# Optimization experiments

Hardware: AMD Instinct MI355X
Metric: run time of the kernel (lower is better)

The kernel has to match this reference:

```python
import jax, jax.numpy as jnp
import numpy as np

N, E, B, D = 50000, 800000, 250, 128
EPS = 1e-5


def setup_inputs() -> dict:
    key = jax.random.key(0)
    ks = jax.random.split(key, 12)
    x = jax.random.normal(ks[0], (N, D), jnp.float32)
    w = jax.random.uniform(ks[1], (E, 4), jnp.float32)
    src = jax.random.randint(ks[2], (E,), 0, N)
    dst = jax.random.randint(ks[3], (E,), 0, N)
    graph_ids = jnp.sort(jax.random.randint(ks[4], (N,), 0, B))
    s = 1.0 / np.sqrt(D)
    W1 = jax.random.normal(ks[5], (D, D), jnp.float32) * s
    W2 = jax.random.normal(ks[6], (D, D), jnp.float32) * s
    W3 = jax.random.normal(ks[7], (D, D), jnp.float32) * s
    ln1_g = jnp.ones((D,), jnp.float32)
    ln1_b = jnp.zeros((D,), jnp.float32)
    ln2_g = jnp.ones((D,), jnp.float32)
    ln2_b = jnp.zeros((D,), jnp.float32)
    return dict(x=x, w=w, W1=W1, W2=W2, W3=W3, ln1_g=ln1_g, ln1_b=ln1_b,
                ln2_g=ln2_g, ln2_b=ln2_b, src=src, dst=dst, graph_ids=graph_ids)


def _layernorm(h, g, b):
    mu = jnp.mean(h, axis=-1, keepdims=True)
    var = jnp.mean(jnp.square(h - mu), axis=-1, keepdims=True)
    return (h - mu) * jax.lax.rsqrt(var + EPS) * g + b


def reference(x, w, W1, W2, W3, ln1_g, ln1_b, ln2_g, ln2_b, src, dst, graph_ids):
    # edge feature [E,Fe] -> scalar edge weight [E] (mean over feature dim)
    w_s = jnp.mean(w, axis=-1)
    ones_e = jnp.ones((E,), x.dtype)
    # DGL norm='both': unweighted degrees, clamped to >= 1
    out_deg = jnp.clip(jax.ops.segment_sum(ones_e, src, num_segments=N), 1.0)
    in_deg = jnp.clip(jax.ops.segment_sum(ones_e, dst, num_segments=N), 1.0)
    out_norm = jax.lax.rsqrt(out_deg)[:, None]  # [N,1]
    in_norm = jax.lax.rsqrt(in_deg)[:, None]    # [N,1]

    def gconv(h, W):
        m = (h * out_norm)[src] * w_s[:, None]                 # [E,D] gather-mul
        agg = jax.ops.segment_sum(m, dst, num_segments=N)      # [N,D] scatter-add
        return (agg * in_norm) @ W                              # [N,D_out]

    h = _layernorm(jax.nn.relu(gconv(x, W1)), ln1_g, ln1_b)
    h = _layernorm(jax.nn.relu(gconv(h, W2)), ln2_g, ln2_b)
    h = gconv(h, W3)
    # per-graph segmented sum readout -> [B, D]
    return jax.ops.segment_sum(h, graph_ids, num_segments=B)
```

## Files before the change

kernel.cpp:

```cpp
#include <hip/hip_runtime.h>

#define D 128
#define RS 16
#define NBMAX 1024
constexpr float EPS = 1e-5f;

typedef short bf16x8 __attribute__((ext_vector_type(8)));
typedef float f32x4 __attribute__((ext_vector_type(4)));
typedef unsigned long long u64;

__device__ __forceinline__ uint f2bf(float f) {
  union { float f; uint u; } v; v.f = f;
  return (v.u + 0x7fffu + ((v.u >> 16) & 1u)) >> 16;
}
__device__ __forceinline__ float bflo(uint u) {
  union { uint u; float f; } v; v.u = u << 16; return v.f;
}
__device__ __forceinline__ float bfhi(uint u) {
  union { uint u; float f; } v; v.u = u & 0xffff0000u; return v.f;
}

__device__ __forceinline__ int lower_bound(const int* __restrict__ a, int n, int key) {
  int lo = 0, hi = n;
  while (lo < hi) { int m = (lo + hi) >> 1; if (a[m] < key) lo = m + 1; else hi = m; }
  return lo;
}

__global__ __launch_bounds__(256) void k_pre(
    const int* __restrict__ src, const int* __restrict__ dst,
    int* __restrict__ ocnt, int* __restrict__ btot, int E, int nb, int ebA,
    const float4* __restrict__ x, uint4* __restrict__ xb, int n8, int cb,
    const float* __restrict__ W1, const float* __restrict__ W2,
    const float* __restrict__ W3, ushort* __restrict__ Wf) {
  __shared__ int hloc[NBMAX];
  int bid = blockIdx.x;
  int tid = threadIdx.x;
  if (bid < ebA) {
    for (int j = tid; j < nb; j += 256) hloc[j] = 0;
    __syncthreads();
    int e0 = bid * 4096;
#pragma unroll 4
    for (int it = 0; it < 16; ++it) {
      int e = e0 + it * 256 + tid;
      if (e < E) {
        atomicAdd(&ocnt[src[e]], 1);
        atomicAdd(&hloc[dst[e] >> 6], 1);
      }
    }
    __syncthreads();
    for (int j = tid; j < nb; j += 256) {
      int c = hloc[j];
      if (c) atomicAdd(&btot[j], c);
    }
  } else if (bid < ebA + cb) {
    int i = (bid - ebA) * 256 + tid;
    if (i < n8) {
      float4 p = x[i * 2], q = x[i * 2 + 1];
      uint4 o;
      o.x = f2bf(p.x) | (f2bf(p.y) << 16);
      o.y = f2bf(p.z) | (f2bf(p.w) << 16);
      o.z = f2bf(q.x) | (f2bf(q.y) << 16);
      o.w = f2bf(q.z) | (f2bf(q.w) << 16);
      xb[i] = o;
    }
  } else {
    int t4 = (bid - ebA - cb) * 256 + tid;
    if (t4 < 3 * 2048) {
      const float* Wsrc = (t4 < 2048) ? W1 : (t4 < 4096) ? W2 : W3;
      int t = t4 & 2047;
      int lane = t & 63;
      int frag = t >> 6;
      int ks = frag >> 3, ct = frag & 7;
      int col = ct * 16 + (lane & 15);
      int kb = ks * 32 + (lane >> 4) * 8;
      uint p[8];
#pragma unroll
      for (int j = 0; j < 8; ++j) p[j] = f2bf(Wsrc[(kb + j) * D + col]);
      uint4 o;
      o.x = p[0] | (p[1] << 16);
      o.y = p[2] | (p[3] << 16);
      o.z = p[4] | (p[5] << 16);
      o.w = p[6] | (p[7] << 16);
      *(uint4*)(Wf + (size_t)t4 * 8) = o;
    }
  }
}

__global__ void k_onorm(const int* __restrict__ ocnt, float* __restrict__ outn, int N) {
  int n = blockIdx.x * 256 + threadIdx.x;
  if (n < N) outn[n] = rsqrtf(fmaxf((float)ocnt[n], 1.0f));
}

__global__ __launch_bounds__(1024) void k_bbase(const int* __restrict__ btot,
                                                int* __restrict__ bb,
                                                int* __restrict__ rowptr,
                                                int nb, int E, int N) {
  __shared__ int part[1024];
  int t = threadIdx.x;
  int v = (t < nb) ? btot[t] : 0;
  part[t] = v;
  __syncthreads();
  for (int off = 1; off < 1024; off <<= 1) {
    int u = (t >= off) ? part[t - off] : 0;
    __syncthreads();
    part[t] += u;
    __syncthreads();
  }
  if (t < nb) bb[t] = part[t] - v;
  if (t == 0) { bb[nb] = E; rowptr[N] = E; }
}

__global__ __launch_bounds__(256) void k_bscatter(
    const int* __restrict__ src, const int* __restrict__ dst,
    const float4* __restrict__ w, const float* __restrict__ outn,
    const int* __restrict__ bb, int* __restrict__ bcur,
    u64* __restrict__ ebuf, int E, int nb) {
  __shared__ int hloc[NBMAX];
  __shared__ int hcur[NBMAX];
  int bid = blockIdx.x, tid = threadIdx.x;
  for (int j = tid; j < nb; j += 256) hloc[j] = 0;
  __syncthreads();
  int e0 = bid * 4096;
#pragma unroll 4
  for (int it = 0; it < 16; ++it) {
    int e = e0 + it * 256 + tid;
    if (e < E) atomicAdd(&hloc[dst[e] >> 6], 1);
  }
  __syncthreads();
  for (int j = tid; j < nb; j += 256) {
    int c = hloc[j];
    hcur[j] = c ? (bb[j] + atomicAdd(&bcur[j], c)) : 0;
  }
  __syncthreads();
#pragma unroll 4
  for (int it = 0; it < 16; ++it) {
    int e = e0 + it * 256 + tid;
    if (e < E) {
      int d = dst[e], s = src[e];
      int pos = atomicAdd(&hcur[d >> 6], 1);
      float4 wv = w[e];
      float coef = (wv.x + wv.y + wv.z + wv.w) * 0.25f * outn[s];
      u64 pk = ((u64)__float_as_uint(coef) << 32) |
               ((u64)(d & 63) << 16) | (uint)s;
      ebuf[pos] = pk;
    }
  }
}

__global__ __launch_bounds__(256) void k_bplace(
    const u64* __restrict__ ebuf, const int* __restrict__ bb,
    int* __restrict__ rowptr, float* __restrict__ innm,
    u64* __restrict__ ecsr, int N) {
  __shared__ int c64[64], ex[64], cur[64];
  int b = blockIdx.x, tid = threadIdx.x;
  int base = bb[b];
  int cnt = bb[b + 1] - base;
  if (tid < 64) c64[tid] = 0;
  __syncthreads();
  for (int i = tid; i < cnt; i += 256) {
    u64 v = ebuf[base + i];
    atomicAdd(&c64[(int)((v >> 16) & 63)], 1);
  }
  __syncthreads();
  if (tid < 64) {
    int cv = c64[tid];
    int inc = cv;
#pragma unroll
    for (int off = 1; off < 64; off <<= 1) {
      int u = __shfl_up(inc, off);
      if (tid >= off) inc += u;
    }
    int excl = inc - cv;
    ex[tid] = excl;
    cur[tid] = 0;
    int node = b * 64 + tid;
    if (node < N) {
      rowptr[node] = base + excl;
      innm[node] = rsqrtf(fmaxf((float)cv, 1.0f));
    }
  }
  __syncthreads();
  for (int i = tid; i < cnt; i += 256) {
    u64 v = ebuf[base + i];
    int dl = (int)((v >> 16) & 63);
    int pos = base + ex[dl] + atomicAdd(&cur[dl], 1);
    ecsr[pos] = (v & 0xFFFFFFFF00000000ull) | (v & 0xFFFFull);
  }
}

__global__ __launch_bounds__(256) void k_fused(
    const ushort* __restrict__ h, const int* __restrict__ rowptr,
    const u64* __restrict__ ecsr,
    const float* __restrict__ innm, const ushort* __restrict__ Wf,
    const float* __restrict__ g, const float* __restrict__ bta,
    void* __restrict__ out, int N, int do_ln) {
  __shared__ float lds[4][16 * D];
  const int lane = threadIdx.x & 63;
  const int wv = threadIdx.x >> 6;
  const int row0 = blockIdx.x * 64 + wv * 16;
  if (row0 >= N) return;

  ushort* at = (ushort*)&lds[wv][0];
  {
    const int grp = lane >> 4;
    const int c = lane & 15;
    for (int rr = 0; rr < 4; ++rr) {
      int n = row0 + grp * 4 + rr;
      if (n >= N) break;
      int beg = rowptr[n], end = rowptr[n + 1];
      float a0 = 0, a1 = 0, a2 = 0, a3 = 0, a4 = 0, a5 = 0, a6 = 0, a7 = 0;
#define ACC8(q, f)                                          \
  a0 = fmaf(bflo(q.x), f, a0); a1 = fmaf(bfhi(q.x), f, a1); \
  a2 = fmaf(bflo(q.y), f, a2); a3 = fmaf(bfhi(q.y), f, a3); \
  a4 = fmaf(bflo(q.z), f, a4); a5 = fmaf(bfhi(q.z), f, a5); \
  a6 = fmaf(bflo(q.w), f, a6); a7 = fmaf(bfhi(q.w), f, a7);
      int j = beg;
      for (; j + 4 <= end; j += 4) {
        u64 v0 = ecsr[j], v1 = ecsr[j + 1], v2 = ecsr[j + 2], v3 = ecsr[j + 3];
        const ushort* p0 = h + (size_t)(v0 & 0xFFFFu) * D + c * 8;
        const ushort* p1 = h + (size_t)(v1 & 0xFFFFu) * D + c * 8;
        const ushort* p2 = h + (size_t)(v2 & 0xFFFFu) * D + c * 8;
        const ushort* p3 = h + (size_t)(v3 & 0xFFFFu) * D + c * 8;
        float f0 = __uint_as_float((uint)(v0 >> 32));
        float f1 = __uint_as_float((uint)(v1 >> 32));
        float f2 = __uint_as_float((uint)(v2 >> 32));
        float f3 = __uint_as_float((uint)(v3 >> 32));
        uint4 q0 = *(const uint4*)p0;
        uint4 q1 = *(const uint4*)p1;
        uint4 q2 = *(const uint4*)p2;
        uint4 q3 = *(const uint4*)p3;
        ACC8(q0, f0) ACC8(q1, f1) ACC8(q2, f2) ACC8(q3, f3)
      }
      for (; j < end; ++j) {
        u64 v = ecsr[j];
        float f = __uint_as_float((uint)(v >> 32));
        uint4 q = *(const uint4*)(h + (size_t)(v & 0xFFFFu) * D + c * 8);
        ACC8(q, f)
      }
#undef ACC8
      float sc = innm[n];
      uint4 o;
      o.x = f2bf(a0 * sc) | (f2bf(a1 * sc) << 16);
      o.y = f2bf(a2 * sc) | (f2bf(a3 * sc) << 16);
      o.z = f2bf(a4 * sc) | (f2bf(a5 * sc) << 16);
      o.w = f2bf(a6 * sc) | (f2bf(a7 * sc) << 16);
      *(uint4*)(at + (grp * 4 + rr) * 136 + c * 8) = o;
    }
  }
  asm volatile("s_waitcnt lgkmcnt(0)" ::: "memory");
  __builtin_amdgcn_sched_barrier(0);

  const int lc = lane & 15, lg = lane >> 4;
  f32x4 acc[8];
#pragma unroll
  for (int ct = 0; ct < 8; ++ct) acc[ct] = (f32x4){0.f, 0.f, 0.f, 0.f};
#pragma unroll
  for (int ks = 0; ks < 4; ++ks) {
    bf16x8 a = *(const bf16x8*)(at + lc * 136 + ks * 32 + lg * 8);
    const ushort* wp = Wf + ((size_t)(ks * 8) * 64 + lane) * 8;
#pragma unroll
    for (int ct = 0; ct < 8; ++ct) {
      bf16x8 b = *(const bf16x8*)(wp + ct * 512);
      acc[ct] = __builtin_amdgcn_mfma_f32_16x16x32_bf16(a, b, acc[ct], 0, 0, 0);
    }
  }
  asm volatile("s_waitcnt lgkmcnt(0)" ::: "memory");
  __builtin_amdgcn_sched_barrier(0);

  if (do_ln) {
    float v[8][4];
#pragma unroll
    for (int ct = 0; ct < 8; ++ct)
#pragma unroll
      for (int j = 0; j < 4; ++j) v[ct][j] = fmaxf(acc[ct][j], 0.f);
    float mu[4], rs[4];
#pragma unroll
    for (int j = 0; j < 4; ++j) {
      float s = 0.f;
#pragma unroll
      for (int ct = 0; ct < 8; ++ct) s += v[ct][j];
#pragma unroll
      for (int off = 1; off < 16; off <<= 1) s += __shfl_xor(s, off);
      mu[j] = s * (1.0f / D);
    }
#pragma unroll
    for (int j = 0; j < 4; ++j) {
      float q = 0.f;
#pragma unroll
      for (int ct = 0; ct < 8; ++ct) {
        v[ct][j] -= mu[j];
        q = fmaf(v[ct][j], v[ct][j], q);
      }
#pragma unroll
      for (int off = 1; off < 16; off <<= 1) q += __shfl_xor(q, off);
      rs[j] = rsqrtf(q * (1.0f / D) + EPS);
    }
    ushort* lp = (ushort*)&lds[wv][0];
#pragma unroll
    for (int ct = 0; ct < 8; ++ct) {
      float gc = g[ct * 16 + lc], bc = bta[ct * 16 + lc];
#pragma unroll
      for (int j = 0; j < 4; ++j)
        lp[(lg * 4 + j) * D + ct * 16 + lc] = (ushort)f2bf(fmaf(v[ct][j] * rs[j], gc, bc));
    }
    __builtin_amdgcn_wave_barrier();
    int r = row0 + (lane >> 2);
    if (r < N) {
      ushort* ob = (ushort*)out + (size_t)row0 * D + lane * 32;
#pragma unroll
      for (int i = 0; i < 4; ++i)
        ((uint4*)ob)[i] = ((const uint4*)(lp + lane * 32))[i];
    }
  } else {
    float* lp = &lds[wv][0];
#pragma unroll
    for (int ct = 0; ct < 8; ++ct)
#pragma unroll
      for (int j = 0; j < 4; ++j)
        lp[(lg * 4 + j) * D + ct * 16 + lc] = acc[ct][j];
    __builtin_amdgcn_wave_barrier();
    int r = row0 + (lane >> 2);
    if (r < N) {
      float* ob = (float*)out + (size_t)row0 * D + lane * 32;
#pragma unroll
      for (int i = 0; i < 8; ++i)
        ((float4*)ob)[i] = ((const float4*)(lp + lane * 32))[i];
    }
  }
}

__global__ __launch_bounds__(128) void k_rpart(
    const float* __restrict__ h, const int* __restrict__ gid,
    float* __restrict__ part, int N) {
  int b = blockIdx.x / RS, s = blockIdx.x % RS;
  int t = threadIdx.x;
  int start = lower_bound(gid, N, b);
  int end = lower_bound(gid, N, b + 1);
  int len = end - start;
  int chunk = (len + RS - 1) / RS;
  int rb = start + s * chunk;
  int re = min(rb + chunk, end);
  float acc = 0.f;
  for (int n = rb; n < re; ++n) acc += h[(size_t)n * D + t];
  part[((size_t)b * RS + s) * D + t] = acc;
}

__global__ __launch_bounds__(128) void k_rsum(
    const float* __restrict__ part, float* __restrict__ out) {
  int b = blockIdx.x;
  int t = threadIdx.x;
  float acc = 0.f;
#pragma unroll
  for (int s = 0; s < RS; ++s) acc += part[((size_t)b * RS + s) * D + t];
  out[(size_t)b * D + t] = acc;
}

extern "C" void kernel_launch(void* const* d_in, const int* in_sizes, int n_in,
                              void* d_out, int out_size, void* d_ws, size_t ws_size,
                              hipStream_t stream) {
  const float* x    = (const float*)d_in[0];
  const float* w    = (const float*)d_in[1];
  const float* W1   = (const float*)d_in[2];
  const float* W2   = (const float*)d_in[3];
  const float* W3   = (const float*)d_in[4];
  const float* ln1g = (const float*)d_in[5];
  const float* ln1b = (const float*)d_in[6];
  const float* ln2g = (const float*)d_in[7];
  const float* ln2b = (const float*)d_in[8];
  const int* src = (const int*)d_in[9];
  const int* dst = (const int*)d_in[10];
  const int* gid = (const int*)d_in[11];
  const int N = in_sizes[0] / D;
  const int E = in_sizes[9];
  const int B = out_size / D;
  float* outp = (float*)d_out;

  float*  h3f  = (float*)d_ws;
  ushort* xb   = (ushort*)(h3f + (size_t)N * D);
  ushort* hb1  = xb + (size_t)N * D;
  ushort* Wf   = hb1 + (size_t)N * D;
  float*  outn = (float*)(Wf + 3 * 2048 * 8);
  float*  innm = outn + N;
  const int nb  = (N + 63) >> 6;
  const int ebA = (E + 4095) / 4096;
  int*    ocnt = (int*)(innm + N);
  int*    btot = ocnt + N;
  int*    bcur = btot + nb;
  int*    rowptr = bcur + nb;
  int*    bb   = rowptr + N + 2;
  u64*    ecsr = (u64*)(bb + nb + 2);
  float*  part = (float*)(ecsr + E);
  u64*    ebuf = (u64*)h3f;

  const int mb  = (N + 63) / 64;
  const int n8  = N * D / 8;
  const int cb  = (n8 + 255) / 256;

  hipMemsetAsync(ocnt, 0, sizeof(int) * ((size_t)N + 2 * nb), stream);
  k_pre<<<ebA + cb + 24, 256, 0, stream>>>(src, dst, ocnt, btot, E, nb, ebA,
                                           (const float4*)x, (uint4*)xb, n8, cb,
                                           W1, W2, W3, Wf);
  k_onorm<<<(N + 255) / 256, 256, 0, stream>>>(ocnt, outn, N);
  k_bbase<<<1, 1024, 0, stream>>>(btot, bb, rowptr, nb, E, N);
  k_bscatter<<<ebA, 256, 0, stream>>>(src, dst, (const float4*)w, outn, bb, bcur,
                                      ebuf, E, nb);
  k_bplace<<<nb, 256, 0, stream>>>(ebuf, bb, rowptr, innm, ecsr, N);

  k_fused<<<mb, 256, 0, stream>>>(xb, rowptr, ecsr, innm, Wf,
                                  ln1g, ln1b, hb1, N, 1);
  k_fused<<<mb, 256, 0, stream>>>(hb1, rowptr, ecsr, innm, Wf + 16384,
                                  ln2g, ln2b, xb, N, 1);
  k_fused<<<mb, 256, 0, stream>>>(xb, rowptr, ecsr, innm, Wf + 32768,
                                  nullptr, nullptr, h3f, N, 0);

  k_rpart<<<B * RS, 128, 0, stream>>>(h3f, gid, part, N);
  k_rsum<<<B, 128, 0, stream>>>(part, outp);
}
```

Baseline: 221.4 us.

## Replace global out-degree atomics with bucketed source histogram and per-bucket counting

Out-degrees were counted with 800K global atomics on per-node counters. Now source IDs are bucketed by node>>6 using LDS histograms, the same way destinations are. A second scatter writes the bucketed source IDs and a new k_scount kernel counts them per node in LDS. The out-norm multiply moves from k_bscatter into k_bplace. This removes contended global atomics and the k_onorm launch, but adds an extra scatter pass of 3.2MB, another kernel and a second prefix scan.

```diff
diff --git a/kernel.cpp b/kernel.cpp
--- a/kernel.cpp
+++ b/kernel.cpp
@@ -28,29 +28,32 @@
 
 __global__ __launch_bounds__(256) void k_pre(
     const int* __restrict__ src, const int* __restrict__ dst,
-    int* __restrict__ ocnt, int* __restrict__ btot, int E, int nb, int ebA,
+    int* __restrict__ btot, int* __restrict__ btot2, int E, int nb, int ebA,
     const float4* __restrict__ x, uint4* __restrict__ xb, int n8, int cb,
     const float* __restrict__ W1, const float* __restrict__ W2,
     const float* __restrict__ W3, ushort* __restrict__ Wf) {
-  __shared__ int hloc[NBMAX];
+  __shared__ int hd[NBMAX];
+  __shared__ int hs[NBMAX];
   int bid = blockIdx.x;
   int tid = threadIdx.x;
   if (bid < ebA) {
-    for (int j = tid; j < nb; j += 256) hloc[j] = 0;
+    for (int j = tid; j < nb; j += 256) { hd[j] = 0; hs[j] = 0; }
     __syncthreads();
     int e0 = bid * 4096;
 #pragma unroll 4
     for (int it = 0; it < 16; ++it) {
       int e = e0 + it * 256 + tid;
       if (e < E) {
-        atomicAdd(&ocnt[src[e]], 1);
-        atomicAdd(&hloc[dst[e] >> 6], 1);
+        atomicAdd(&hd[dst[e] >> 6], 1);
+        atomicAdd(&hs[src[e] >> 6], 1);
       }
     }
     __syncthreads();
     for (int j = tid; j < nb; j += 256) {
-      int c = hloc[j];
-      if (c) atomicAdd(&btot[j], c);
+      int cd = hd[j];
+      if (cd) atomicAdd(&btot[j], cd);
+      int cs = hs[j];
+      if (cs) atomicAdd(&btot2[j], cs);
     }
   } else if (bid < ebA + cb) {
     int i = (bid - ebA) * 256 + tid;
@@ -86,15 +89,10 @@
   }
 }
 
-__global__ void k_onorm(const int* __restrict__ ocnt, float* __restrict__ outn, int N) {
-  int n = blockIdx.x * 256 + threadIdx.x;
-  if (n < N) outn[n] = rsqrtf(fmaxf((float)ocnt[n], 1.0f));
-}
-
-__global__ __launch_bounds__(1024) void k_bbase(const int* __restrict__ btot,
-                                                int* __restrict__ bb,
-                                                int* __restrict__ rowptr,
-                                                int nb, int E, int N) {
+__global__ __launch_bounds__(1024) void k_bbase(
+    const int* __restrict__ btot, const int* __restrict__ btot2,
+    int* __restrict__ bb, int* __restrict__ bb2,
+    int* __restrict__ rowptr, int nb, int E, int N) {
   __shared__ int part[1024];
   int t = threadIdx.x;
   int v = (t < nb) ? btot[t] : 0;
@@ -108,28 +106,46 @@
   }
   if (t < nb) bb[t] = part[t] - v;
   if (t == 0) { bb[nb] = E; rowptr[N] = E; }
+  __syncthreads();
+  int v2 = (t < nb) ? btot2[t] : 0;
+  part[t] = v2;
+  __syncthreads();
+  for (int off = 1; off < 1024; off <<= 1) {
+    int u = (t >= off) ? part[t - off] : 0;
+    __syncthreads();
+    part[t] += u;
+    __syncthreads();
+  }
+  if (t < nb) bb2[t] = part[t] - v2;
+  if (t == 0) bb2[nb] = E;
 }
 
 __global__ __launch_bounds__(256) void k_bscatter(
     const int* __restrict__ src, const int* __restrict__ dst,
-    const float4* __restrict__ w, const float* __restrict__ outn,
+    const float4* __restrict__ w,
     const int* __restrict__ bb, int* __restrict__ bcur,
-    u64* __restrict__ ebuf, int E, int nb) {
-  __shared__ int hloc[NBMAX];
-  __shared__ int hcur[NBMAX];
+    const int* __restrict__ bb2, int* __restrict__ bcur2,
+    u64* __restrict__ ebuf, uint* __restrict__ ebuf2, int E, int nb) {
+  __shared__ int hd[NBMAX], hdc[NBMAX];
+  __shared__ int hsv[NBMAX], hsc[NBMAX];
   int bid = blockIdx.x, tid = threadIdx.x;
-  for (int j = tid; j < nb; j += 256) hloc[j] = 0;
+  for (int j = tid; j < nb; j += 256) { hd[j] = 0; hsv[j] = 0; }
   __syncthreads();
   int e0 = bid * 4096;
 #pragma unroll 4
   for (int it = 0; it < 16; ++it) {
     int e = e0 + it * 256 + tid;
-    if (e < E) atomicAdd(&hloc[dst[e] >> 6], 1);
+    if (e < E) {
+      atomicAdd(&hd[dst[e] >> 6], 1);
+      atomicAdd(&hsv[src[e] >> 6], 1);
+    }
   }
   __syncthreads();
   for (int j = tid; j < nb; j += 256) {
-    int c = hloc[j];
-    hcur[j] = c ? (bb[j] + atomicAdd(&bcur[j], c)) : 0;
+    int cd = hd[j];
+    hdc[j] = cd ? (bb[j] + atomicAdd(&bcur[j], cd)) : 0;
+    int cs = hsv[j];
+    hsc[j] = cs ? (bb2[j] + atomicAdd(&bcur2[j], cs)) : 0;
   }
   __syncthreads();
 #pragma unroll 4
@@ -137,18 +153,39 @@
     int e = e0 + it * 256 + tid;
     if (e < E) {
       int d = dst[e], s = src[e];
-      int pos = atomicAdd(&hcur[d >> 6], 1);
+      int pos = atomicAdd(&hdc[d >> 6], 1);
       float4 wv = w[e];
-      float coef = (wv.x + wv.y + wv.z + wv.w) * 0.25f * outn[s];
-      u64 pk = ((u64)__float_as_uint(coef) << 32) |
+      float meanw = (wv.x + wv.y + wv.z + wv.w) * 0.25f;
+      u64 pk = ((u64)__float_as_uint(meanw) << 32) |
                ((u64)(d & 63) << 16) | (uint)s;
       ebuf[pos] = pk;
-    }
+      int pos2 = atomicAdd(&hsc[s >> 6], 1);
+      ebuf2[pos2] = (uint)s;
+    }
+  }
+}
+
+__global__ __launch_bounds__(256) void k_scount(
+    const uint* __restrict__ ebuf2, const int* __restrict__ bb2,
+    float* __restrict__ outn, int N) {
+  __shared__ int c64[64];
+  int b = blockIdx.x, tid = threadIdx.x;
+  int base = bb2[b];
+  int cnt = bb2[b + 1] - base;
+  if (tid < 64) c64[tid] = 0;
+  __syncthreads();
+  for (int i = tid; i < cnt; i += 256)
+    atomicAdd(&c64[ebuf2[base + i] & 63], 1);
+  __syncthreads();
+  if (tid < 64) {
+    int node = b * 64 + tid;
+    if (node < N) outn[node] = rsqrtf(fmaxf((float)c64[tid], 1.0f));
   }
 }
 
 __global__ __launch_bounds__(256) void k_bplace(
     const u64* __restrict__ ebuf, const int* __restrict__ bb,
+    const float* __restrict__ outn,
     int* __restrict__ rowptr, float* __restrict__ innm,
     u64* __restrict__ ecsr, int N) {
   __shared__ int c64[64], ex[64], cur[64];
@@ -183,8 +220,10 @@
   for (int i = tid; i < cnt; i += 256) {
     u64 v = ebuf[base + i];
     int dl = (int)((v >> 16) & 63);
+    int s = (int)(v & 0xFFFFu);
+    float coef = __uint_as_float((uint)(v >> 32)) * outn[s];
     int pos = base + ex[dl] + atomicAdd(&cur[dl], 1);
-    ecsr[pos] = (v & 0xFFFFFFFF00000000ull) | (v & 0xFFFFull);
+    ecsr[pos] = ((u64)__float_as_uint(coef) << 32) | (uint)s;
   }
 }
 
@@ -383,28 +422,31 @@
   float*  innm = outn + N;
   const int nb  = (N + 63) >> 6;
   const int ebA = (E + 4095) / 4096;
-  int*    ocnt = (int*)(innm + N);
-  int*    btot = ocnt + N;
+  int*    btot = (int*)(innm + N);
   int*    bcur = btot + nb;
-  int*    rowptr = bcur + nb;
+  int*    btot2= bcur + nb;
+  int*    bcur2= btot2 + nb;
+  int*    rowptr = bcur2 + nb;
   int*    bb   = rowptr + N + 2;
-  u64*    ecsr = (u64*)(bb + nb + 2);
+  int*    bb2  = bb + nb + 2;
+  u64*    ecsr = (u64*)(bb2 + nb + 2);
   float*  part = (float*)(ecsr + E);
   u64*    ebuf = (u64*)h3f;
+  uint*   ebuf2= (uint*)(ebuf + E);
 
   const int mb  = (N + 63) / 64;
   const int n8  = N * D / 8;
   const int cb  = (n8 + 255) / 256;
 
-  hipMemsetAsync(ocnt, 0, sizeof(int) * ((size_t)N + 2 * nb), stream);
-  k_pre<<<ebA + cb + 24, 256, 0, stream>>>(src, dst, ocnt, btot, E, nb, ebA,
+  hipMemsetAsync(btot, 0, sizeof(int) * (size_t)(4 * nb), stream);
+  k_pre<<<ebA + cb + 24, 256, 0, stream>>>(src, dst, btot, btot2, E, nb, ebA,
                                            (const float4*)x, (uint4*)xb, n8, cb,
                                            W1, W2, W3, Wf);
-  k_onorm<<<(N + 255) / 256, 256, 0, stream>>>(ocnt, outn, N);
-  k_bbase<<<1, 1024, 0, stream>>>(btot, bb, rowptr, nb, E, N);
-  k_bscatter<<<ebA, 256, 0, stream>>>(src, dst, (const float4*)w, outn, bb, bcur,
-                                      ebuf, E, nb);
-  k_bplace<<<nb, 256, 0, stream>>>(ebuf, bb, rowptr, innm, ecsr, N);
+  k_bbase<<<1, 1024, 0, stream>>>(btot, btot2, bb, bb2, rowptr, nb, E, N);
+  k_bscatter<<<ebA, 256, 0, stream>>>(src, dst, (const float4*)w, bb, bcur,
+                                      bb2, bcur2, ebuf, ebuf2, E, nb);
+  k_scount<<<nb, 256, 0, stream>>>(ebuf2, bb2, outn, N);
+  k_bplace<<<nb, 256, 0, stream>>>(ebuf, bb, outn, rowptr, innm, ecsr, N);
 
   k_fused<<<mb, 256, 0, stream>>>(xb, rowptr, ecsr, innm, Wf,
                                   ln1g, ln1b, hb1, N, 1);
```

Result: faster. 212.4 us (-4.1%).
